# Optimization experiments

Measured on AMD Instinct MI355X. Metric: run time of the kernel, lower is better.

Reference implementation:

```python
import jax, jax.numpy as jnp
import numpy as np

N_EMBED = 1024
NUM_HEADS = 16
HEAD_SIZE = 64  # NUM_HEADS * HEAD_SIZE == N_EMBED
BLOCK_SIZE = 2048


def setup_inputs() -> dict:
    key = jax.random.key(0)
    ks = jax.random.split(key, 9)
    s = 1.0 / np.sqrt(N_EMBED)
    batch_x = jax.random.normal(ks[0], (4, BLOCK_SIZE, N_EMBED), dtype=jnp.float32)
    # stacked per-head linear params: weight [H, E, d], bias [H, d]
    Wq = jax.random.uniform(ks[1], (NUM_HEADS, N_EMBED, HEAD_SIZE), jnp.float32, -s, s)
    Wk = jax.random.uniform(ks[2], (NUM_HEADS, N_EMBED, HEAD_SIZE), jnp.float32, -s, s)
    Wv = jax.random.uniform(ks[3], (NUM_HEADS, N_EMBED, HEAD_SIZE), jnp.float32, -s, s)
    bq = jax.random.uniform(ks[4], (NUM_HEADS, HEAD_SIZE), jnp.float32, -s, s)
    bk = jax.random.uniform(ks[5], (NUM_HEADS, HEAD_SIZE), jnp.float32, -s, s)
    bv = jax.random.uniform(ks[6], (NUM_HEADS, HEAD_SIZE), jnp.float32, -s, s)
    Wp = jax.random.uniform(ks[7], (N_EMBED, N_EMBED), jnp.float32, -s, s)
    bp = jax.random.uniform(ks[8], (N_EMBED,), jnp.float32, -s, s)
    return {"batch_x": batch_x, "Wq": Wq, "Wk": Wk, "Wv": Wv,
            "bq": bq, "bk": bk, "bv": bv, "Wp": Wp, "bp": bp}


def reference(batch_x, Wq, Wk, Wv, bq, bk, bv, Wp, bp):
    B, T, E = batch_x.shape
    # per-head projections: [B, H, T, d]
    q = jnp.einsum('bte,hed->bhtd', batch_x, Wq) + bq[None, :, None, :]
    k = jnp.einsum('bte,hed->bhtd', batch_x, Wk) + bk[None, :, None, :]
    v = jnp.einsum('bte,hed->bhtd', batch_x, Wv) + bv[None, :, None, :]
    scale = 1.0 / jnp.sqrt(jnp.asarray(HEAD_SIZE, batch_x.dtype))
    wei = jnp.einsum('bhtd,bhsd->bhts', q, k) * scale  # [B,H,T,T]
    causal = jnp.tril(jnp.ones((T, T), dtype=bool))
    wei = jnp.where(causal, wei, jnp.asarray(-jnp.inf, wei.dtype))
    wei = jax.nn.softmax(wei, axis=-1)
    out = jnp.einsum('bhts,bhsd->bhtd', wei, v)  # [B,H,T,d]
    # concat heads (head order matches torch.cat over ModuleList)
    out = out.transpose(0, 2, 1, 3).reshape(B, T, NUM_HEADS * HEAD_SIZE)
    return out @ Wp + bp
```

## Files before the change

### kernel.cpp

```cpp
#include <hip/hip_runtime.h>
#include <math.h>

#define B_ 4
#define T_ 2048
#define E_ 1024
#define H_ 16
#define D_ 64

typedef __bf16 bf16_t;
typedef bf16_t bf16x8 __attribute__((ext_vector_type(8)));
typedef float  f32x4  __attribute__((ext_vector_type(4)));
typedef float  f32x16 __attribute__((ext_vector_type(16)));
typedef unsigned short u16x4 __attribute__((ext_vector_type(4)));
typedef unsigned int   u32x4 __attribute__((ext_vector_type(4)));

static __device__ __forceinline__ unsigned short f2bf(float f) {
    bf16_t h = (bf16_t)f;
    return __builtin_bit_cast(unsigned short, h);
}
static __device__ __forceinline__ unsigned int pk2(float a, float b) {
    return (unsigned int)f2bf(a) | ((unsigned int)f2bf(b) << 16);
}
static __device__ __forceinline__ float ex2(float x) {
    float r; asm("v_exp_f32 %0, %1" : "=v"(r) : "v"(x)); return r;
}
static __device__ __forceinline__ void pl32swap(unsigned int& a, unsigned int& b) {
    asm("v_permlane32_swap_b32 %0, %1" : "+v"(a), "+v"(b));
}

#define GLD(gp, lp) __builtin_amdgcn_global_load_lds( \
    (const __attribute__((address_space(1))) unsigned int*)(gp), \
    (__attribute__((address_space(3))) unsigned int*)(lp), 16, 0, 0)

#define BAR() __builtin_amdgcn_s_barrier()
#define WAIT_LGKM0() asm volatile("s_waitcnt lgkmcnt(0)" ::: "memory")
#define VMC(n) asm volatile("s_waitcnt vmcnt(" #n ")" ::: "memory")

__global__ void prep_kernel(const float* __restrict__ xin, unsigned short* __restrict__ xb,
                            const float* __restrict__ Wq, const float* __restrict__ Wk,
                            const float* __restrict__ Wv, const float* __restrict__ Wp,
                            unsigned short* __restrict__ wf, unsigned short* __restrict__ wpt) {
    __shared__ unsigned short Ts[64 * 66];
    const int bid = blockIdx.x;
    const int tid = threadIdx.x;
    if (bid < 8192) {
        int i = bid * 256 + tid;
        float4 v = ((const float4*)xin)[i];
        ushort4 o;
        o.x = f2bf(v.x); o.y = f2bf(v.y); o.z = f2bf(v.z); o.w = f2bf(v.w);
        ((ushort4*)xb)[i] = o;
        return;
    }
    const int b2 = bid - 8192;
    const int bx = b2 & 15, by = b2 >> 4;
    const int grp = by >> 4, yy = by & 15;
    const float* in; unsigned short* out; int yA, S;
    if (grp == 3) { in = Wp; out = wpt; yA = 64;    S = 1024; }
    else {
        in = (grp == 0) ? Wq : (grp == 1) ? Wk : Wv;
        out = wf + (size_t)grp * 1024 * 1024; yA = 65536; S = 64;
    }
    const int r = tid >> 2, c4 = tid & 3;
    const float* ip = in + (size_t)yA * yy + (size_t)(bx * 64 + r) * S + c4 * 16;
    #pragma unroll
    for (int j = 0; j < 4; ++j) {
        float4 v = *(const float4*)&ip[j * 4];
        Ts[(c4 * 16 + j * 4 + 0) * 66 + r] = f2bf(v.x);
        Ts[(c4 * 16 + j * 4 + 1) * 66 + r] = f2bf(v.y);
        Ts[(c4 * 16 + j * 4 + 2) * 66 + r] = f2bf(v.z);
        Ts[(c4 * 16 + j * 4 + 3) * 66 + r] = f2bf(v.w);
    }
    __syncthreads();
    unsigned short* op = out + (size_t)(yy * 64 + r) * 1024 + bx * 64 + c4 * 16;
    #pragma unroll
    for (int j = 0; j < 4; ++j) {
        u16x4 pk;
        #pragma unroll
        for (int m = 0; m < 4; ++m) pk[m] = Ts[r * 66 + c4 * 16 + j * 4 + m];
        *(u16x4*)&op[j * 4] = pk;
    }
}


#define GEMM_CORE_DECLS \
    const int tid = threadIdx.x; \
    const int w = tid >> 6, lane = tid & 63; \
    const int wr = w >> 2, wc = w & 3; \
    const int l15 = lane & 15, quad = lane >> 4, lsw = l15 & 7; \
    const int rowg = lane >> 3; \
    const int swz = ((lane & 7) ^ rowg) * 8; \
    f32x4 acc[4][4]; \
    _Pragma("unroll") for (int i_ = 0; i_ < 4; ++i_) \
        _Pragma("unroll") for (int j_ = 0; j_ < 4; ++j_) \
            acc[i_][j_] = (f32x4){0.f, 0.f, 0.f, 0.f};

#define MFMA_P(nb) \
    __builtin_amdgcn_s_setprio(1); \
    _Pragma("unroll") for (int m_ = 0; m_ < 4; ++m_) \
        _Pragma("unroll") for (int j_ = 0; j_ < 2; ++j_) \
            _Pragma("unroll") for (int k_ = 0; k_ < 2; ++k_) \
                acc[m_][(nb) + j_] = __builtin_amdgcn_mfma_f32_16x16x32_bf16( \
                    fA[m_][k_], fB[(nb) + j_][k_], acc[m_][(nb) + j_], 0, 0, 0); \
    __builtin_amdgcn_s_setprio(0);

#define GEMM_K_LOOP \
    stageA(0, 0); stageA(0, 1); stageB(0, 0, 0); stageB(0, 0, 1); \
    stageB(0, 1, 0); stageB(0, 1, 1); \
    stageA(1, 0); stageA(1, 1); stageB(1, 0, 0); stageB(1, 0, 1); \
    VMC(6); BAR(); \
    _Pragma("unroll 1") \
    for (int it = 0; it < 8; ++it) { \
        const int t0 = 2 * it, t1 = 2 * it + 1; \
        const bool more = it < 7; \
        bf16x8 fA[4][2], fB[4][2]; \
         \
        _Pragma("unroll") for (int m_ = 0; m_ < 4; ++m_) { fA[m_][0] = rdA(t0, m_, 0); fA[m_][1] = rdA(t0, m_, 1); } \
        _Pragma("unroll") for (int n_ = 0; n_ < 2; ++n_) { fB[n_][0] = rdB(t0, n_, 0); fB[n_][1] = rdB(t0, n_, 1); } \
        stageB(t1, 1, 0); stageB(t1, 1, 1); \
        BAR(); WAIT_LGKM0(); \
        MFMA_P(0); \
        VMC(6); BAR(); \
         \
        _Pragma("unroll") for (int n_ = 0; n_ < 2; ++n_) { fB[2 + n_][0] = rdB(t0, 2 + n_, 0); fB[2 + n_][1] = rdB(t0, 2 + n_, 1); } \
        if (more) { stageA(t0 + 2, 0); stageA(t0 + 2, 1); stageB(t0 + 2, 0, 0); stageB(t0 + 2, 0, 1); } \
        BAR(); WAIT_LGKM0(); \
        MFMA_P(2); \
        if (more) { VMC(6); } else { VMC(2); } \
        BAR(); \
         \
        _Pragma("unroll") for (int m_ = 0; m_ < 4; ++m_) { fA[m_][0] = rdA(t1, m_, 0); fA[m_][1] = rdA(t1, m_, 1); } \
        _Pragma("unroll") for (int n_ = 0; n_ < 2; ++n_) { fB[n_][0] = rdB(t1, n_, 0); fB[n_][1] = rdB(t1, n_, 1); } \
        if (more) { stageB(t0 + 2, 1, 0); stageB(t0 + 2, 1, 1); } \
        BAR(); WAIT_LGKM0(); \
        MFMA_P(0); \
        if (more) { VMC(6); } else { VMC(0); } \
        BAR(); \
         \
        _Pragma("unroll") for (int n_ = 0; n_ < 2; ++n_) { fB[2 + n_][0] = rdB(t1, 2 + n_, 0); fB[2 + n_][1] = rdB(t1, 2 + n_, 1); } \
        if (more) { stageA(t1 + 2, 0); stageA(t1 + 2, 1); stageB(t1 + 2, 0, 0); stageB(t1 + 2, 0, 1); } \
        BAR(); WAIT_LGKM0(); \
        MFMA_P(2); \
        if (more) { VMC(6); } \
        BAR(); \
    }

__global__ __launch_bounds__(512, 2) void qkv_gemm(
    const unsigned short* __restrict__ xb,
    const unsigned short* __restrict__ wf,
    const float* __restrict__ bq, const float* __restrict__ bk, const float* __restrict__ bv,
    unsigned short* __restrict__ qo, unsigned short* __restrict__ ko,
    unsigned short* __restrict__ vt)
{
    __shared__ __align__(16) unsigned short sm[49152];

    const int bid = blockIdx.x;
    const int m0 = (bid & 63) * 128;
    const int n0 = (bid >> 6) * 256;

    GEMM_CORE_DECLS

    auto stageA = [&](int t, int g) {
        const int rb = w * 16 + g * 8;
        unsigned short* dst = sm + (t & 1) * 24576 + rb * 64;
        GLD(xb + (size_t)(m0 + rb + rowg) * 1024 + t * 64 + swz, dst);
    };
    auto stageB = [&](int t, int R, int g) {
        const int rb = w * 16 + g * 8;
        const int ar0 = (rb >> 5) * 64 + R * 32 + (rb & 31);
        unsigned short* dst = sm + (t & 1) * 24576 + 8192 + ar0 * 64;
        GLD(wf + (size_t)(n0 + ar0 + rowg) * 1024 + t * 64 + swz, dst);
    };
    auto rdA = [&](int t, int fm, int ks) {
        const int row = wr * 64 + fm * 16 + l15;
        return *(const bf16x8*)&sm[(t & 1) * 24576 + row * 64 + (((ks * 4 + quad) ^ lsw) * 8)];
    };
    auto rdB = [&](int t, int fn, int ks) {
        const int row = wc * 64 + fn * 16 + l15;
        return *(const bf16x8*)&sm[(t & 1) * 24576 + 8192 + row * 64 + (((ks * 4 + quad) ^ lsw) * 8)];
    };

    GEMM_K_LOOP

    const int which = n0 >> 10;
    const int nb = n0 & 1023;
    if (which < 2) {
        const float* bias = which ? bk : bq;
        unsigned short* outp = which ? ko : qo;
        const float sc = which ? 1.f : 0.125f * 1.44269504088896f;
        #pragma unroll
        for (int fm = 0; fm < 4; ++fm)
            #pragma unroll
            for (int fn = 0; fn < 4; ++fn) {
                int colg = nb + wc * 64 + fn * 16 + l15;
                int h = colg >> 6, d = colg & 63;
                float bi = bias[colg];
                #pragma unroll
                for (int r = 0; r < 4; ++r) {
                    int row = m0 + wr * 64 + fm * 16 + quad * 4 + r;
                    int b = row >> 11, t = row & 2047;
                    outp[(((size_t)b * 16 + h) * 2048 + t) * 64 + d] = f2bf((acc[fm][fn][r] + bi) * sc);
                }
            }
    } else {
        const int b = m0 >> 11, t0r = m0 & 2047;
        for (int nh = 0; nh < 2; ++nh) {
            __syncthreads();
            if ((wc >> 1) == nh) {
                const int cc = wc & 1;
                #pragma unroll
                for (int fm = 0; fm < 4; ++fm)
                    #pragma unroll
                    for (int fn = 0; fn < 4; ++fn) {
                        int colL = cc * 64 + fn * 16 + l15;
                        int colg = nb + nh * 128 + colL;
                        float bi = bv[colg];
                        u16x4 pk;
                        #pragma unroll
                        for (int r = 0; r < 4; ++r) pk[r] = f2bf(acc[fm][fn][r] + bi);
                        *(u16x4*)&sm[colL * 136 + wr * 64 + fm * 16 + quad * 4] = pk;
                    }
            }
            __syncthreads();
            const int nl = tid >> 2, tq = tid & 3;
            const int colg = nb + nh * 128 + nl;
            const int h = colg >> 6, d = colg & 63;
            unsigned short* dst = vt + (((size_t)b * 16 + h) * 64 + d) * 2048 + t0r + tq * 32;
            #pragma unroll
            for (int j = 0; j < 4; ++j)
                *(float4*)&dst[j * 8] = *(const float4*)&sm[nl * 136 + tq * 32 + j * 8];
        }
    }
}

__global__ __launch_bounds__(512, 2) void proj_gemm(
    const unsigned short* __restrict__ A,
    const unsigned short* __restrict__ wpt,
    const float* __restrict__ bp,
    float* __restrict__ out)
{
    __shared__ __align__(16) unsigned short sm[49152];

    const int bid = blockIdx.x;
    const int m0 = (bid & 63) * 128;
    const int n0 = (bid >> 6) * 256;

    GEMM_CORE_DECLS

    const unsigned short* Ab = A + (size_t)(m0 >> 11) * 16 * 131072 + (size_t)(m0 & 2047) * 64;
    auto stageA = [&](int t, int g) {
        const int rb = w * 16 + g * 8;
        unsigned short* dst = sm + (t & 1) * 24576 + rb * 64;
        GLD(Ab + (size_t)t * 131072 + (rb + rowg) * 64 + swz, dst);
    };
    auto stageB = [&](int t, int R, int g) {
        const int rb = w * 16 + g * 8;
        const int ar0 = (rb >> 5) * 64 + R * 32 + (rb & 31);
        unsigned short* dst = sm + (t & 1) * 24576 + 8192 + ar0 * 64;
        GLD(wpt + (size_t)(n0 + ar0 + rowg) * 1024 + t * 64 + swz, dst);
    };
    auto rdA = [&](int t, int fm, int ks) {
        const int row = wr * 64 + fm * 16 + l15;
        return *(const bf16x8*)&sm[(t & 1) * 24576 + row * 64 + (((ks * 4 + quad) ^ lsw) * 8)];
    };
    auto rdB = [&](int t, int fn, int ks) {
        const int row = wc * 64 + fn * 16 + l15;
        return *(const bf16x8*)&sm[(t & 1) * 24576 + 8192 + row * 64 + (((ks * 4 + quad) ^ lsw) * 8)];
    };

    GEMM_K_LOOP

    #pragma unroll
    for (int fm = 0; fm < 4; ++fm)
        #pragma unroll
        for (int fn = 0; fn < 4; ++fn) {
            int col = n0 + wc * 64 + fn * 16 + l15;
            float bi = bp[col];
            #pragma unroll
            for (int r = 0; r < 4; ++r) {
                int row = m0 + wr * 64 + fm * 16 + quad * 4 + r;
                out[(size_t)row * 1024 + col] = acc[fm][fn][r] + bi;
            }
        }
}

__global__ __launch_bounds__(512, 4) void attn_kernel(
    const unsigned short* __restrict__ q, const unsigned short* __restrict__ k,
    const unsigned short* __restrict__ vt, unsigned short* __restrict__ att2)
{
    __shared__ __align__(16) unsigned short KV[2][2][4096];

    const int tid = threadIdx.x;
    const int w = tid >> 6, lane = tid & 63;
    const int l31 = lane & 31, h = lane >> 5;
    const int qg2 = w >> 1, ksel = w & 1;
    const int bh = blockIdx.x;
    const int rs = l31 & 7;

    const unsigned short* kb = k  + (size_t)bh * 2048 * 64;
    const unsigned short* vb = vt + (size_t)bh * 64 * 2048;

    u32x4 onesu; onesu[0] = onesu[1] = onesu[2] = onesu[3] = 0x3F803F80u;
    const bf16x8 bOnes = __builtin_bit_cast(bf16x8, onesu);

    const int rg = lane >> 3;
    const size_t kOff = (size_t)(8 * w + rg) * 64 + (size_t)(((lane & 7) ^ rg) * 8);
    const size_t vOff = (size_t)(8 * w + rg) * 2048 + (size_t)(((lane & 7) ^ rg) * 8);

    auto stage = [&](int jt, int buf) {
        GLD(kb + kOff + (size_t)jt * 4096, &KV[buf][0][w * 512]);
        GLD(vb + vOff + jt * 64,           &KV[buf][1][w * 512]);
    };

    for (int leg = 0; leg < 2; ++leg) {
        const int qtile = leg ? (15 - (int)blockIdx.y) : (int)blockIdx.y;
        const int qb0 = qtile * 128;
        const int qmin = qb0 + qg2 * 32, qmax = qmin + 31;
        const int qg = qmin + l31;
        const int trips = 2 * qtile + 2;

        bf16x8 fQ[4];
        {
            const unsigned short* qp = q + ((size_t)bh * 2048 + qg) * 64 + h * 8;
            #pragma unroll
            for (int ks = 0; ks < 4; ++ks) fQ[ks] = *(const bf16x8*)&qp[ks * 16];
        }

        f32x16 O[2], Osum;
        #pragma unroll
        for (int nt = 0; nt < 2; ++nt)
            #pragma unroll
            for (int i = 0; i < 16; ++i) O[nt][i] = 0.f;
        #pragma unroll
        for (int i = 0; i < 16; ++i) Osum[i] = 0.f;

        stage(0, 0);
        VMC(0);
        BAR();

        for (int jt = 0; jt < trips; ++jt) {
            const int buf = jt & 1;
            if (jt + 1 < trips) stage(jt + 1, buf ^ 1);
            const unsigned short* Ks = KV[buf][0];
            const unsigned short* Vs = KV[buf][1];
            const int wk0 = jt * 64 + 32 * ksel;

            if (wk0 <= qmax) {
                f32x16 S;
                #pragma unroll
                for (int i = 0; i < 16; ++i) S[i] = 0.f;
                __builtin_amdgcn_s_setprio(1);
                {
                    const int row = 32 * ksel + l31;
                    #pragma unroll
                    for (int ks = 0; ks < 4; ++ks) {
                        bf16x8 aK = *(const bf16x8*)&Ks[row * 64 + (((2 * ks + h) ^ rs) * 8)];
                        S = __builtin_amdgcn_mfma_f32_32x32x16_bf16(aK, fQ[ks], S, 0, 0, 0);
                    }
                }
                __builtin_amdgcn_s_setprio(0);

                const bool nm = (wk0 + 31) > qmin;
                unsigned int e0[4], e1[4];
                #pragma unroll
                for (int g = 0; g < 4; ++g) {
                    float p[4];
                    #pragma unroll
                    for (int r = 0; r < 4; ++r) {
                        float pv = ex2(S[4 * g + r]);
                        if (nm) {
                            int key = wk0 + 8 * g + 4 * h + r;
                            if (key > qg) pv = 0.f;
                        }
                        p[r] = pv;
                    }
                    e0[g] = pk2(p[0], p[1]);
                    e1[g] = pk2(p[2], p[3]);
                }

                __builtin_amdgcn_s_setprio(1);
                #pragma unroll
                for (int s = 0; s < 2; ++s) {
                    unsigned int a = e0[2 * s], b = e0[2 * s + 1];
                    pl32swap(a, b);
                    unsigned int c2 = e1[2 * s], d2 = e1[2 * s + 1];
                    pl32swap(c2, d2);
                    u32x4 t; t[0] = a; t[1] = c2; t[2] = b; t[3] = d2;
                    bf16x8 aP = __builtin_bit_cast(bf16x8, t);
                    const int cb = 4 * ksel + 2 * s;
                    #pragma unroll
                    for (int nt = 0; nt < 2; ++nt) {
                        const int drow = nt * 32 + l31;
                        bf16x8 bV = *(const bf16x8*)&Vs[drow * 64 + (((cb + h) ^ rs) * 8)];
                        O[nt] = __builtin_amdgcn_mfma_f32_32x32x16_bf16(aP, bV, O[nt], 0, 0, 0);
                    }
                    Osum = __builtin_amdgcn_mfma_f32_32x32x16_bf16(aP, bOnes, Osum, 0, 0, 0);
                }
                __builtin_amdgcn_s_setprio(0);
            }

            VMC(0);
            BAR();
        }

        float* Lf = (float*)KV;
        for (int half = 0; half < 2; ++half) {
            __syncthreads();
            float* mb = Lf + (size_t)(qg2 & 1) * 48 * 64;
            if ((qg2 >> 1) == half && ksel) {
                #pragma unroll
                for (int nt = 0; nt < 2; ++nt)
                    #pragma unroll
                    for (int i = 0; i < 16; ++i)
                        mb[(nt * 16 + i) * 64 + lane] = O[nt][i];
                #pragma unroll
                for (int i = 0; i < 16; ++i)
                    mb[(32 + i) * 64 + lane] = Osum[i];
            }
            __syncthreads();
            if ((qg2 >> 1) == half && !ksel) {
                #pragma unroll
                for (int nt = 0; nt < 2; ++nt)
                    #pragma unroll
                    for (int i = 0; i < 16; ++i)
                        O[nt][i] += mb[(nt * 16 + i) * 64 + lane];
                #pragma unroll
                for (int i = 0; i < 16; ++i)
                    Osum[i] += mb[(32 + i) * 64 + lane];

                unsigned short* ob = att2 + ((size_t)bh * 2048 + qmin) * 64;
                #pragma unroll
                for (int g = 0; g < 4; ++g)
                    #pragma unroll
                    for (int r = 0; r < 4; ++r) {
                        const float iv = 1.f / Osum[4 * g + r];
                        const int qy = 8 * g + 4 * h + r;
                        #pragma unroll
                        for (int nt = 0; nt < 2; ++nt)
                            ob[(size_t)qy * 64 + nt * 32 + l31] = f2bf(O[nt][4 * g + r] * iv);
                    }
            }
        }
        __syncthreads();
    }
}

extern "C" void kernel_launch(void* const* d_in, const int* in_sizes, int n_in,
                              void* d_out, int out_size, void* d_ws, size_t ws_size,
                              hipStream_t stream) {
    const float* x  = (const float*)d_in[0];
    const float* Wq = (const float*)d_in[1];
    const float* Wk = (const float*)d_in[2];
    const float* Wv = (const float*)d_in[3];
    const float* bq = (const float*)d_in[4];
    const float* bk = (const float*)d_in[5];
    const float* bv = (const float*)d_in[6];
    const float* Wp = (const float*)d_in[7];
    const float* bp = (const float*)d_in[8];
    float* out = (float*)d_out;

    const size_t nx = (size_t)B_ * T_ * E_;
    unsigned short* base = (unsigned short*)d_ws;
    unsigned short* xb  = base;
    unsigned short* qb  = xb + nx;
    unsigned short* kb  = qb + nx;
    unsigned short* vtb = kb + nx;
    unsigned short* atb = vtb + nx;
    unsigned short* wf  = atb + nx;
    unsigned short* wpt = wf + 3072 * 1024;

    prep_kernel<<<9216, 256, 0, stream>>>(x, xb, Wq, Wk, Wv, Wp, wf, wpt);
    qkv_gemm<<<768, 512, 0, stream>>>(xb, wf, bq, bk, bv, qb, kb, vtb);
    attn_kernel<<<dim3(64, 8), 512, 0, stream>>>(qb, kb, vtb, atb);
    proj_gemm<<<256, 512, 0, stream>>>(atb, wpt, bp, out);
}
```

Measured before the change: 253.2 us.

## Rewrite QKV GEMM main loop with K-tile 32 and halved shared memory

The QKV projection GEMM now stages K tiles of 32 instead of 64, cutting its shared-memory buffer from 96KB to 48KB and using a simpler 4-chunk XOR swizzle. The main loop runs 32 iterations with two MFMA phases per tile, prefetching A one tile ahead and B two tiles ahead. The intent is lower LDS footprint, which may allow more resident blocks, and a simpler pipeline. The cost is twice as many barriers per unit of K work and less latency hiding per iteration. The shared GEMM macros are moved below so proj_gemm still uses the original loop.

```diff
diff --git a/kernel.cpp b/kernel.cpp
--- a/kernel.cpp
+++ b/kernel.cpp
@@ -81,69 +81,6 @@
     }
 }
 
-
-#define GEMM_CORE_DECLS \
-    const int tid = threadIdx.x; \
-    const int w = tid >> 6, lane = tid & 63; \
-    const int wr = w >> 2, wc = w & 3; \
-    const int l15 = lane & 15, quad = lane >> 4, lsw = l15 & 7; \
-    const int rowg = lane >> 3; \
-    const int swz = ((lane & 7) ^ rowg) * 8; \
-    f32x4 acc[4][4]; \
-    _Pragma("unroll") for (int i_ = 0; i_ < 4; ++i_) \
-        _Pragma("unroll") for (int j_ = 0; j_ < 4; ++j_) \
-            acc[i_][j_] = (f32x4){0.f, 0.f, 0.f, 0.f};
-
-#define MFMA_P(nb) \
-    __builtin_amdgcn_s_setprio(1); \
-    _Pragma("unroll") for (int m_ = 0; m_ < 4; ++m_) \
-        _Pragma("unroll") for (int j_ = 0; j_ < 2; ++j_) \
-            _Pragma("unroll") for (int k_ = 0; k_ < 2; ++k_) \
-                acc[m_][(nb) + j_] = __builtin_amdgcn_mfma_f32_16x16x32_bf16( \
-                    fA[m_][k_], fB[(nb) + j_][k_], acc[m_][(nb) + j_], 0, 0, 0); \
-    __builtin_amdgcn_s_setprio(0);
-
-#define GEMM_K_LOOP \
-    stageA(0, 0); stageA(0, 1); stageB(0, 0, 0); stageB(0, 0, 1); \
-    stageB(0, 1, 0); stageB(0, 1, 1); \
-    stageA(1, 0); stageA(1, 1); stageB(1, 0, 0); stageB(1, 0, 1); \
-    VMC(6); BAR(); \
-    _Pragma("unroll 1") \
-    for (int it = 0; it < 8; ++it) { \
-        const int t0 = 2 * it, t1 = 2 * it + 1; \
-        const bool more = it < 7; \
-        bf16x8 fA[4][2], fB[4][2]; \
-         \
-        _Pragma("unroll") for (int m_ = 0; m_ < 4; ++m_) { fA[m_][0] = rdA(t0, m_, 0); fA[m_][1] = rdA(t0, m_, 1); } \
-        _Pragma("unroll") for (int n_ = 0; n_ < 2; ++n_) { fB[n_][0] = rdB(t0, n_, 0); fB[n_][1] = rdB(t0, n_, 1); } \
-        stageB(t1, 1, 0); stageB(t1, 1, 1); \
-        BAR(); WAIT_LGKM0(); \
-        MFMA_P(0); \
-        VMC(6); BAR(); \
-         \
-        _Pragma("unroll") for (int n_ = 0; n_ < 2; ++n_) { fB[2 + n_][0] = rdB(t0, 2 + n_, 0); fB[2 + n_][1] = rdB(t0, 2 + n_, 1); } \
-        if (more) { stageA(t0 + 2, 0); stageA(t0 + 2, 1); stageB(t0 + 2, 0, 0); stageB(t0 + 2, 0, 1); } \
-        BAR(); WAIT_LGKM0(); \
-        MFMA_P(2); \
-        if (more) { VMC(6); } else { VMC(2); } \
-        BAR(); \
-         \
-        _Pragma("unroll") for (int m_ = 0; m_ < 4; ++m_) { fA[m_][0] = rdA(t1, m_, 0); fA[m_][1] = rdA(t1, m_, 1); } \
-        _Pragma("unroll") for (int n_ = 0; n_ < 2; ++n_) { fB[n_][0] = rdB(t1, n_, 0); fB[n_][1] = rdB(t1, n_, 1); } \
-        if (more) { stageB(t0 + 2, 1, 0); stageB(t0 + 2, 1, 1); } \
-        BAR(); WAIT_LGKM0(); \
-        MFMA_P(0); \
-        if (more) { VMC(6); } else { VMC(0); } \
-        BAR(); \
-         \
-        _Pragma("unroll") for (int n_ = 0; n_ < 2; ++n_) { fB[2 + n_][0] = rdB(t1, 2 + n_, 0); fB[2 + n_][1] = rdB(t1, 2 + n_, 1); } \
-        if (more) { stageA(t1 + 2, 0); stageA(t1 + 2, 1); stageB(t1 + 2, 0, 0); stageB(t1 + 2, 0, 1); } \
-        BAR(); WAIT_LGKM0(); \
-        MFMA_P(2); \
-        if (more) { VMC(6); } \
-        BAR(); \
-    }
-
 __global__ __launch_bounds__(512, 2) void qkv_gemm(
     const unsigned short* __restrict__ xb,
     const unsigned short* __restrict__ wf,
@@ -151,35 +88,78 @@
     unsigned short* __restrict__ qo, unsigned short* __restrict__ ko,
     unsigned short* __restrict__ vt)
 {
-    __shared__ __align__(16) unsigned short sm[49152];
-
-    const int bid = blockIdx.x;
-    const int m0 = (bid & 63) * 128;
-    const int n0 = (bid >> 6) * 256;
-
-    GEMM_CORE_DECLS
-
-    auto stageA = [&](int t, int g) {
-        const int rb = w * 16 + g * 8;
-        unsigned short* dst = sm + (t & 1) * 24576 + rb * 64;
-        GLD(xb + (size_t)(m0 + rb + rowg) * 1024 + t * 64 + swz, dst);
-    };
-    auto stageB = [&](int t, int R, int g) {
-        const int rb = w * 16 + g * 8;
-        const int ar0 = (rb >> 5) * 64 + R * 32 + (rb & 31);
-        unsigned short* dst = sm + (t & 1) * 24576 + 8192 + ar0 * 64;
-        GLD(wf + (size_t)(n0 + ar0 + rowg) * 1024 + t * 64 + swz, dst);
-    };
-    auto rdA = [&](int t, int fm, int ks) {
+    __shared__ __align__(16) unsigned short sm[24576];
+
+    const int tid = threadIdx.x;
+    const int w = tid >> 6, lane = tid & 63;
+    const int wr = w >> 2, wc = w & 3;
+    const int l15 = lane & 15, quad = lane >> 4;
+    const int lsw3 = l15 & 3;
+    const int m0 = (blockIdx.x & 63) * 128;
+    const int n0 = (blockIdx.x >> 6) * 256;
+
+    f32x4 acc[4][4];
+    #pragma unroll
+    for (int i = 0; i < 4; ++i)
+        #pragma unroll
+        for (int j = 0; j < 4; ++j) acc[i][j] = (f32x4){0.f, 0.f, 0.f, 0.f};
+
+    const int arow = tid >> 2;
+    const int achk = (tid & 3) ^ (arow & 3);
+    const unsigned short* Agb = xb + (size_t)(m0 + arow) * 1024 + achk * 8;
+    const unsigned short* Bgb0 = wf + (size_t)(n0 + arow) * 1024 + achk * 8;
+    const unsigned short* Bgb1 = wf + (size_t)(n0 + 128 + arow) * 1024 + achk * 8;
+
+    auto stageA = [&](int t) {
+        GLD(Agb + t * 32, sm + (t & 1) * 12288 + tid * 8);
+    };
+    auto stageB = [&](int t, int half) {
+        GLD((half ? Bgb1 : Bgb0) + t * 32,
+            sm + (t & 1) * 12288 + 4096 + (half * 512 + tid) * 8);
+    };
+    auto rdA = [&](int t, int fm) {
         const int row = wr * 64 + fm * 16 + l15;
-        return *(const bf16x8*)&sm[(t & 1) * 24576 + row * 64 + (((ks * 4 + quad) ^ lsw) * 8)];
-    };
-    auto rdB = [&](int t, int fn, int ks) {
+        return *(const bf16x8*)&sm[(t & 1) * 12288 + row * 32 + ((quad ^ lsw3) * 8)];
+    };
+    auto rdB = [&](int t, int fn) {
         const int row = wc * 64 + fn * 16 + l15;
-        return *(const bf16x8*)&sm[(t & 1) * 24576 + 8192 + row * 64 + (((ks * 4 + quad) ^ lsw) * 8)];
-    };
-
-    GEMM_K_LOOP
+        return *(const bf16x8*)&sm[(t & 1) * 12288 + 4096 + row * 32 + ((quad ^ lsw3) * 8)];
+    };
+
+    stageA(0); stageB(0, 0); stageB(0, 1);
+    stageA(1); stageB(1, 0); stageB(1, 1);
+    VMC(3); BAR();
+
+    #pragma unroll 1
+    for (int t = 0; t < 32; ++t) {
+        bf16x8 fB[4], fA0, fA1;
+        #pragma unroll
+        for (int n = 0; n < 4; ++n) fB[n] = rdB(t, n);
+        fA0 = rdA(t, 0); fA1 = rdA(t, 1);
+        if (t >= 1 && t < 31) stageA(t + 1);
+        BAR(); WAIT_LGKM0();
+        __builtin_amdgcn_s_setprio(1);
+        #pragma unroll
+        for (int n = 0; n < 4; ++n) {
+            acc[0][n] = __builtin_amdgcn_mfma_f32_16x16x32_bf16(fA0, fB[n], acc[0][n], 0, 0, 0);
+            acc[1][n] = __builtin_amdgcn_mfma_f32_16x16x32_bf16(fA1, fB[n], acc[1][n], 0, 0, 0);
+        }
+        __builtin_amdgcn_s_setprio(0);
+        BAR();
+
+        fA0 = rdA(t, 2); fA1 = rdA(t, 3);
+        if (t < 30) { stageB(t + 2, 0); stageB(t + 2, 1); }
+        BAR(); WAIT_LGKM0();
+        __builtin_amdgcn_s_setprio(1);
+        #pragma unroll
+        for (int n = 0; n < 4; ++n) {
+            acc[2][n] = __builtin_amdgcn_mfma_f32_16x16x32_bf16(fA0, fB[n], acc[2][n], 0, 0, 0);
+            acc[3][n] = __builtin_amdgcn_mfma_f32_16x16x32_bf16(fA1, fB[n], acc[3][n], 0, 0, 0);
+        }
+        __builtin_amdgcn_s_setprio(0);
+        if (t < 30) { VMC(2); } else if (t == 30) { VMC(0); }
+        BAR();
+    }
 
     const int which = n0 >> 10;
     const int nb = n0 & 1023;
@@ -232,6 +212,65 @@
     }
 }
 
+
+#define GEMM_CORE_DECLS \
+    const int tid = threadIdx.x; \
+    const int w = tid >> 6, lane = tid & 63; \
+    const int wr = w >> 2, wc = w & 3; \
+    const int l15 = lane & 15, quad = lane >> 4, lsw = l15 & 7; \
+    const int rowg = lane >> 3; \
+    const int swz = ((lane & 7) ^ rowg) * 8; \
+    f32x4 acc[4][4]; \
+    _Pragma("unroll") for (int i_ = 0; i_ < 4; ++i_) \
+        _Pragma("unroll") for (int j_ = 0; j_ < 4; ++j_) \
+            acc[i_][j_] = (f32x4){0.f, 0.f, 0.f, 0.f};
+
+#define MFMA_P(nb) \
+    __builtin_amdgcn_s_setprio(1); \
+    _Pragma("unroll") for (int m_ = 0; m_ < 4; ++m_) \
+        _Pragma("unroll") for (int j_ = 0; j_ < 2; ++j_) \
+            _Pragma("unroll") for (int k_ = 0; k_ < 2; ++k_) \
+                acc[m_][(nb) + j_] = __builtin_amdgcn_mfma_f32_16x16x32_bf16( \
+                    fA[m_][k_], fB[(nb) + j_][k_], acc[m_][(nb) + j_], 0, 0, 0); \
+    __builtin_amdgcn_s_setprio(0);
+
+#define GEMM_K_LOOP \
+    stageA(0, 0); stageA(0, 1); stageB(0, 0, 0); stageB(0, 0, 1); \
+    stageB(0, 1, 0); stageB(0, 1, 1); \
+    stageA(1, 0); stageA(1, 1); stageB(1, 0, 0); stageB(1, 0, 1); \
+    VMC(6); BAR(); \
+    _Pragma("unroll 1") \
+    for (int it = 0; it < 8; ++it) { \
+        const int t0 = 2 * it, t1 = 2 * it + 1; \
+        const bool more = it < 7; \
+        bf16x8 fA[4][2], fB[4][2]; \
+        _Pragma("unroll") for (int m_ = 0; m_ < 4; ++m_) { fA[m_][0] = rdA(t0, m_, 0); fA[m_][1] = rdA(t0, m_, 1); } \
+        _Pragma("unroll") for (int n_ = 0; n_ < 2; ++n_) { fB[n_][0] = rdB(t0, n_, 0); fB[n_][1] = rdB(t0, n_, 1); } \
+        stageB(t1, 1, 0); stageB(t1, 1, 1); \
+        BAR(); WAIT_LGKM0(); \
+        MFMA_P(0); \
+        VMC(6); BAR(); \
+        _Pragma("unroll") for (int n_ = 0; n_ < 2; ++n_) { fB[2 + n_][0] = rdB(t0, 2 + n_, 0); fB[2 + n_][1] = rdB(t0, 2 + n_, 1); } \
+        if (more) { stageA(t0 + 2, 0); stageA(t0 + 2, 1); stageB(t0 + 2, 0, 0); stageB(t0 + 2, 0, 1); } \
+        BAR(); WAIT_LGKM0(); \
+        MFMA_P(2); \
+        if (more) { VMC(6); } else { VMC(2); } \
+        BAR(); \
+        _Pragma("unroll") for (int m_ = 0; m_ < 4; ++m_) { fA[m_][0] = rdA(t1, m_, 0); fA[m_][1] = rdA(t1, m_, 1); } \
+        _Pragma("unroll") for (int n_ = 0; n_ < 2; ++n_) { fB[n_][0] = rdB(t1, n_, 0); fB[n_][1] = rdB(t1, n_, 1); } \
+        if (more) { stageB(t0 + 2, 1, 0); stageB(t0 + 2, 1, 1); } \
+        BAR(); WAIT_LGKM0(); \
+        MFMA_P(0); \
+        if (more) { VMC(6); } else { VMC(0); } \
+        BAR(); \
+        _Pragma("unroll") for (int n_ = 0; n_ < 2; ++n_) { fB[2 + n_][0] = rdB(t1, 2 + n_, 0); fB[2 + n_][1] = rdB(t1, 2 + n_, 1); } \
+        if (more) { stageA(t1 + 2, 0); stageA(t1 + 2, 1); stageB(t1 + 2, 0, 0); stageB(t1 + 2, 0, 1); } \
+        BAR(); WAIT_LGKM0(); \
+        MFMA_P(2); \
+        if (more) { VMC(6); } \
+        BAR(); \
+    }
+
 __global__ __launch_bounds__(512, 2) void proj_gemm(
     const unsigned short* __restrict__ A,
     const unsigned short* __restrict__ wpt,
```

Result: faster. 242.9 us (-4.1%).
